# Kernel optimization log

Hardware: AMD Instinct MI355X
Metric: run time of the kernel (lower is better)

Reference implementation:

```python
import jax, jax.numpy as jnp
import numpy as np


def setup_inputs() -> dict:
    key = jax.random.key(0)
    ks = jax.random.split(key, 6)
    B, T, H, L, V = 8, 100, 1024, 512, 32000
    x = jax.random.normal(ks[0], (B, T, H), dtype=jnp.float32)
    attn_dist = jax.random.normal(ks[1], (B, T, L), dtype=jnp.float32)
    enc_input = jax.random.randint(ks[2], (B, L), 0, V, dtype=jnp.int32)
    W_vocab = jax.random.normal(ks[3], (H, V), dtype=jnp.float32) * (1.0 / np.sqrt(H))
    b_vocab = jnp.zeros((V,), dtype=jnp.float32)
    w_gen = jax.random.normal(ks[4], (H, 1), dtype=jnp.float32) * (1.0 / np.sqrt(H))
    b_gen = jnp.zeros((1,), dtype=jnp.float32)
    return {"x": x, "attn_dist": attn_dist, "enc_input": enc_input,
            "W_vocab": W_vocab, "b_vocab": b_vocab, "w_gen": w_gen, "b_gen": b_gen}


def reference(x, attn_dist, enc_input, W_vocab, b_vocab, w_gen, b_gen):
    B, T, H = x.shape
    L = attn_dist.shape[-1]
    V = W_vocab.shape[-1]
    # generation gate: sigmoid(x @ w_gen + b_gen) -> [B, T, 1]
    p_gen = jax.nn.sigmoid(jnp.einsum('bth,ho->bto', x, w_gen) + b_gen)
    # vocab distribution: softmax over vocab of the projection -> [B, T, V]
    vocab_dist = jax.nn.softmax(jnp.einsum('bth,hv->btv', x, W_vocab) + b_vocab, axis=-1)
    vocab_dist = p_gen * vocab_dist
    # copy distribution over encoder positions -> [B, T, L]
    copy_dist = (1.0 - p_gen) * jax.nn.softmax(attn_dist, axis=-1)
    # scatter-add copy probabilities into vocab slots (duplicates accumulate)
    vd = vocab_dist.reshape(B * T, V)
    cd = copy_dist.reshape(B * T, L)
    idx = jnp.broadcast_to(enc_input[:, None, :], (B, T, L)).reshape(B * T, L)
    rows = jnp.arange(B * T, dtype=jnp.int32)[:, None]
    combined = vd.at[rows, idx].add(cd)
    return jnp.log(combined).reshape(B, T, V)
```

## Files before the change

kernel.cpp:

```cpp
#include <hip/hip_runtime.h>
#include <math.h>

#define BB 8
#define TT 100
#define HH 1024
#define LL 512
#define VV 32000
#define NROWS (BB*TT)
#define MPAD 896
#define NMT 7
#define NNT 250
#define NWG (NMT*NNT)

typedef __bf16 bf16x8 __attribute__((ext_vector_type(8)));
typedef __bf16 bf16x4 __attribute__((ext_vector_type(4)));
typedef float f32x4 __attribute__((ext_vector_type(4)));

__device__ __forceinline__ void gload16(const void* g, void* l) {
  __builtin_amdgcn_global_load_lds(
      (const __attribute__((address_space(1))) unsigned int*)g,
      (__attribute__((address_space(3))) unsigned int*)l, 16, 0, 0);
}

__global__ __launch_bounds__(256) void k_cvt_x(const float* __restrict__ x,
                                               __bf16* __restrict__ xb) {
  int idx = blockIdx.x * 256 + threadIdx.x;
  int row = (idx * 4) >> 10;
  bf16x4 v;
  if (row < NROWS) {
    float4 f = ((const float4*)x)[idx];
    v[0] = (__bf16)f.x; v[1] = (__bf16)f.y; v[2] = (__bf16)f.z; v[3] = (__bf16)f.w;
  } else {
    v[0] = v[1] = v[2] = v[3] = (__bf16)0.f;
  }
  ((bf16x4*)xb)[idx] = v;
}

__global__ __launch_bounds__(256) void k_cvt_wT(const float* __restrict__ W,
                                                __bf16* __restrict__ Wtb) {
  __shared__ float T[32][257];
  int n0 = blockIdx.x * 256;
  int kt = blockIdx.y;
  int tid = threadIdx.x;
#pragma unroll
  for (int i = 0; i < 32; ++i)
    T[i][tid] = W[(size_t)(kt * 32 + i) * VV + n0 + tid];
  __syncthreads();
  int cq = tid & 3;
  int cl = tid >> 2;
  __bf16* base = Wtb + ((size_t)kt * VV + n0) * 32;
#pragma unroll
  for (int g = 0; g < 4; ++g) {
    int col = g * 64 + cl;
    bf16x8 v;
#pragma unroll
    for (int j = 0; j < 8; ++j) v[j] = (__bf16)T[cq * 8 + j][col];
    *(bf16x8*)(base + (size_t)col * 32 + cq * 8) = v;
  }
}

__global__ __launch_bounds__(256) void k_pgen_copy(
    const float* __restrict__ x, const float* __restrict__ attn,
    const float* __restrict__ w_gen, const float* __restrict__ b_gen,
    float* __restrict__ p_gen, float* __restrict__ copy_dist,
    float* __restrict__ rsum) {
  int r = blockIdx.x;
  int tid = threadIdx.x;
  __shared__ float red[4];
  if (tid == 0) rsum[r] = 0.f;

  float d = 0.f;
  for (int h = tid; h < HH; h += 256) d += x[(size_t)r * HH + h] * w_gen[h];
#pragma unroll
  for (int o = 32; o > 0; o >>= 1) d += __shfl_down(d, o, 64);
  if ((tid & 63) == 0) red[tid >> 6] = d;
  __syncthreads();
  float dot = red[0] + red[1] + red[2] + red[3];
  float p = 1.f / (1.f + __expf(-(dot + b_gen[0])));
  if (tid == 0) p_gen[r] = p;

  float a0 = attn[(size_t)r * LL + tid];
  float a1 = attn[(size_t)r * LL + 256 + tid];
  float m = fmaxf(a0, a1);
#pragma unroll
  for (int o = 32; o > 0; o >>= 1) m = fmaxf(m, __shfl_down(m, o, 64));
  __syncthreads();
  if ((tid & 63) == 0) red[tid >> 6] = m;
  __syncthreads();
  float M = fmaxf(fmaxf(red[0], red[1]), fmaxf(red[2], red[3]));
  float e0 = __expf(a0 - M), e1 = __expf(a1 - M);
  float s = e0 + e1;
#pragma unroll
  for (int o = 32; o > 0; o >>= 1) s += __shfl_down(s, o, 64);
  __syncthreads();
  if ((tid & 63) == 0) red[tid >> 6] = s;
  __syncthreads();
  float S = red[0] + red[1] + red[2] + red[3];
  float scale = (1.f - p) / S;
  copy_dist[(size_t)r * LL + tid] = e0 * scale;
  copy_dist[(size_t)r * LL + 256 + tid] = e1 * scale;
}

__global__ __launch_bounds__(256) void k_gemm_mfma(
    const __bf16* __restrict__ Xb, const __bf16* __restrict__ Wtb,
    const float* __restrict__ bias, float* __restrict__ out,
    float* __restrict__ rsum) {
  __shared__ __align__(16) __bf16 As[2][128 * 32];
  __shared__ __align__(16) __bf16 Bs[2][128 * 32];
  int tid = threadIdx.x;
  int lane = tid & 63, wave = tid >> 6;
  int wr = wave >> 1, wc = wave & 1;
  int l15 = lane & 15, quad = lane >> 4;

  int lid = blockIdx.x;
  int xcd = lid & 7, sub = lid >> 3;
  const int q = NWG >> 3, rr = NWG & 7;
  int wg = (xcd < rr) ? (xcd * (q + 1) + sub)
                      : (rr * (q + 1) + (xcd - rr) * q + sub);
  int m0 = (wg % NMT) * 128;
  int n0 = (wg / NMT) * 128;

  f32x4 acc[4][4];
#pragma unroll
  for (int mi = 0; mi < 4; ++mi)
#pragma unroll
    for (int ni = 0; ni < 4; ++ni) acc[mi][ni] = (f32x4){0.f, 0.f, 0.f, 0.f};

  int r0 = wave * 32;
  const __bf16* aptr0 = Xb + (size_t)(m0 + r0 + (lane >> 2)) * HH + (lane & 3) * 8;
  const __bf16* aptr1 = aptr0 + (size_t)16 * HH;
  const size_t bstep = (size_t)VV * 32;
  const __bf16* bptr0 = Wtb + (size_t)(n0 + r0 + (lane >> 2)) * 32 + (lane & 3) * 8;
  const __bf16* bptr1 = bptr0 + (size_t)16 * 32;

  __bf16* lA0[2] = {&As[0][r0 * 32], &As[1][r0 * 32]};
  __bf16* lA1[2] = {&As[0][(r0 + 16) * 32], &As[1][(r0 + 16) * 32]};
  __bf16* lB0[2] = {&Bs[0][r0 * 32], &Bs[1][r0 * 32]};
  __bf16* lB1[2] = {&Bs[0][(r0 + 16) * 32], &Bs[1][(r0 + 16) * 32]};

  gload16(aptr0, lA0[0]);
  gload16(aptr1, lA1[0]);
  gload16(bptr0, lB0[0]);
  gload16(bptr1, lB1[0]);

  for (int it = 0; it < 32; ++it) {
    int cur = it & 1;
    __syncthreads();
    if (it + 1 < 32) {
      int ko = (it + 1) * 32;
      size_t bo = (size_t)(it + 1) * bstep;
      int nxt = cur ^ 1;
      gload16(aptr0 + ko, lA0[nxt]);
      gload16(aptr1 + ko, lA1[nxt]);
      gload16(bptr0 + bo, lB0[nxt]);
      gload16(bptr1 + bo, lB1[nxt]);
    }
    const __bf16* Ab = As[cur];
    const __bf16* Bb = Bs[cur];
    bf16x8 af[4], bfg[4];
#pragma unroll
    for (int mi = 0; mi < 4; ++mi)
      af[mi] = *(const bf16x8*)&Ab[(wr * 64 + mi * 16 + l15) * 32 + quad * 8];
#pragma unroll
    for (int ni = 0; ni < 4; ++ni)
      bfg[ni] = *(const bf16x8*)&Bb[(wc * 64 + ni * 16 + l15) * 32 + quad * 8];
#pragma unroll
    for (int mi = 0; mi < 4; ++mi)
#pragma unroll
      for (int ni = 0; ni < 4; ++ni)
        acc[mi][ni] = __builtin_amdgcn_mfma_f32_16x16x32_bf16(af[mi], bfg[ni], acc[mi][ni], 0, 0, 0);
  }

  float bv4[4];
#pragma unroll
  for (int ni = 0; ni < 4; ++ni) bv4[ni] = bias[n0 + wc * 64 + ni * 16 + l15];

#pragma unroll
  for (int mi = 0; mi < 4; ++mi) {
#pragma unroll
    for (int rg = 0; rg < 4; ++rg) {
      int row = m0 + wr * 64 + mi * 16 + quad * 4 + rg;
      bool valid = row < NROWS;
      float esum = 0.f;
#pragma unroll
      for (int ni = 0; ni < 4; ++ni) {
        int col = n0 + wc * 64 + ni * 16 + l15;
        float v = acc[mi][ni][rg] + bv4[ni];
        if (valid) out[(size_t)row * VV + col] = v;
        esum += __expf(v);
      }
#pragma unroll
      for (int o = 8; o > 0; o >>= 1) esum += __shfl_down(esum, o, 16);
      if (l15 == 0 && valid) atomicAdd(&rsum[row], esum);
    }
  }
}

__global__ __launch_bounds__(256) void k_affine(
    float* __restrict__ out, const float* __restrict__ p_gen,
    const float* __restrict__ rsum) {
  int r = blockIdx.y;
  int c = (blockIdx.x * 256 + threadIdx.x) * 4;
  if (c >= VV) return;
  float logc = __logf(p_gen[r] / rsum[r]);
  float4 v = *(float4*)&out[(size_t)r * VV + c];
  v.x += logc; v.y += logc; v.z += logc; v.w += logc;
  *(float4*)&out[(size_t)r * VV + c] = v;
}

__global__ __launch_bounds__(256) void k_scatter_fix(
    float* __restrict__ out, const int* __restrict__ enc,
    const float* __restrict__ copy) {
  __shared__ int hkey[1024];
  __shared__ float hval[1024];
  int r = blockIdx.x, tid = threadIdx.x;
  float* row = out + (size_t)r * VV;
  for (int i = tid; i < 1024; i += 256) { hkey[i] = -1; hval[i] = 0.f; }
  __syncthreads();
  int b = r / TT;
  for (int j = tid; j < LL; j += 256) {
    int v = enc[(size_t)b * LL + j];
    float cv = copy[(size_t)r * LL + j];
    unsigned h = ((unsigned)v * 2654435761u) & 1023u;
    while (true) {
      int prev = atomicCAS(&hkey[h], -1, v);
      if (prev == -1 || prev == v) { atomicAdd(&hval[h], cv); break; }
      h = (h + 1) & 1023u;
    }
  }
  __syncthreads();
  for (int h = tid; h < 1024; h += 256) {
    int col = hkey[h];
    if (col >= 0) {
      float stored = row[col];
      row[col] = __logf(__expf(stored) + hval[h]);
    }
  }
}

extern "C" void kernel_launch(void* const* d_in, const int* in_sizes, int n_in,
                              void* d_out, int out_size, void* d_ws, size_t ws_size,
                              hipStream_t stream) {
  const float* x    = (const float*)d_in[0];
  const float* attn = (const float*)d_in[1];
  const int*   enc  = (const int*)d_in[2];
  const float* Wv   = (const float*)d_in[3];
  const float* bv   = (const float*)d_in[4];
  const float* wgen = (const float*)d_in[5];
  const float* bg   = (const float*)d_in[6];
  float* out = (float*)d_out;
  float* ws = (float*)d_ws;

  float* p_gen = ws;
  float* rsum  = ws + 1024;
  float* copy  = ws + 2048;
  __bf16* xb = (__bf16*)(ws + 2048 + NROWS * LL);
  __bf16* Wt = (__bf16*)((char*)xb + (size_t)MPAD * HH * 2);

  k_cvt_x<<<MPAD * HH / 4 / 256, 256, 0, stream>>>(x, xb);
  dim3 gw(VV / 256, HH / 32);
  k_cvt_wT<<<gw, 256, 0, stream>>>(Wv, Wt);
  k_pgen_copy<<<NROWS, 256, 0, stream>>>(x, attn, wgen, bg, p_gen, copy, rsum);
  k_gemm_mfma<<<NWG, 256, 0, stream>>>(xb, Wt, bv, out, rsum);
  dim3 ga((VV + 1023) / 1024, NROWS);
  k_affine<<<ga, 256, 0, stream>>>(out, p_gen, rsum);
  k_scatter_fix<<<NROWS, 256, 0, stream>>>(out, enc, copy);
}
```

Measured before the change: 368.6 us.

## Triple-buffer GEMM LDS stages with vmcnt waits and XOR-swizzled LDS layout

Replaces the double-buffered K loop of the MFMA vocab GEMM with a three-stage LDS ring. Two tiles are kept in flight, and explicit s_waitcnt vmcnt plus a barrier wait only for the oldest load. It also XOR-swizzles the 16-byte chunk position in each LDS row on both the global-to-LDS write and the fragment read, to cut bank conflicts. Together these aim to hide global load latency and LDS conflicts, at the cost of 50% more shared memory per block and hand-managed wait counts that must match the load ordering.

```diff
diff --git a/kernel.cpp b/kernel.cpp
--- a/kernel.cpp
+++ b/kernel.cpp
@@ -105,8 +105,8 @@
     const __bf16* __restrict__ Xb, const __bf16* __restrict__ Wtb,
     const float* __restrict__ bias, float* __restrict__ out,
     float* __restrict__ rsum) {
-  __shared__ __align__(16) __bf16 As[2][128 * 32];
-  __shared__ __align__(16) __bf16 Bs[2][128 * 32];
+  __shared__ __align__(16) __bf16 As[3][128 * 32];
+  __shared__ __align__(16) __bf16 Bs[3][128 * 32];
   int tid = threadIdx.x;
   int lane = tid & 63, wave = tid >> 6;
   int wr = wave >> 1, wc = wave & 1;
@@ -127,49 +127,60 @@
     for (int ni = 0; ni < 4; ++ni) acc[mi][ni] = (f32x4){0.f, 0.f, 0.f, 0.f};
 
   int r0 = wave * 32;
-  const __bf16* aptr0 = Xb + (size_t)(m0 + r0 + (lane >> 2)) * HH + (lane & 3) * 8;
+  int lr = lane >> 2;
+  int chunk = (lane & 3) ^ ((lr >> 1) & 3);
+  const __bf16* aptr0 = Xb + (size_t)(m0 + r0 + lr) * HH + chunk * 8;
   const __bf16* aptr1 = aptr0 + (size_t)16 * HH;
   const size_t bstep = (size_t)VV * 32;
-  const __bf16* bptr0 = Wtb + (size_t)(n0 + r0 + (lane >> 2)) * 32 + (lane & 3) * 8;
+  const __bf16* bptr0 = Wtb + (size_t)(n0 + r0 + lr) * 32 + chunk * 8;
   const __bf16* bptr1 = bptr0 + (size_t)16 * 32;
 
-  __bf16* lA0[2] = {&As[0][r0 * 32], &As[1][r0 * 32]};
-  __bf16* lA1[2] = {&As[0][(r0 + 16) * 32], &As[1][(r0 + 16) * 32]};
-  __bf16* lB0[2] = {&Bs[0][r0 * 32], &Bs[1][r0 * 32]};
-  __bf16* lB1[2] = {&Bs[0][(r0 + 16) * 32], &Bs[1][(r0 + 16) * 32]};
-
-  gload16(aptr0, lA0[0]);
-  gload16(aptr1, lA1[0]);
-  gload16(bptr0, lB0[0]);
-  gload16(bptr1, lB1[0]);
-
-  for (int it = 0; it < 32; ++it) {
-    int cur = it & 1;
-    __syncthreads();
-    if (it + 1 < 32) {
-      int ko = (it + 1) * 32;
-      size_t bo = (size_t)(it + 1) * bstep;
-      int nxt = cur ^ 1;
-      gload16(aptr0 + ko, lA0[nxt]);
-      gload16(aptr1 + ko, lA1[nxt]);
-      gload16(bptr0 + bo, lB0[nxt]);
-      gload16(bptr1 + bo, lB1[nxt]);
-    }
-    const __bf16* Ab = As[cur];
-    const __bf16* Bb = Bs[cur];
-    bf16x8 af[4], bfg[4];
-#pragma unroll
-    for (int mi = 0; mi < 4; ++mi)
-      af[mi] = *(const bf16x8*)&Ab[(wr * 64 + mi * 16 + l15) * 32 + quad * 8];
-#pragma unroll
-    for (int ni = 0; ni < 4; ++ni)
-      bfg[ni] = *(const bf16x8*)&Bb[(wc * 64 + ni * 16 + l15) * 32 + quad * 8];
-#pragma unroll
-    for (int mi = 0; mi < 4; ++mi)
-#pragma unroll
-      for (int ni = 0; ni < 4; ++ni)
-        acc[mi][ni] = __builtin_amdgcn_mfma_f32_16x16x32_bf16(af[mi], bfg[ni], acc[mi][ni], 0, 0, 0);
-  }
+  int sw8 = (quad ^ ((l15 >> 1) & 3)) * 8;
+
+#define STAGE(it, buf) do {                                          \
+    gload16(aptr0 + (size_t)(it) * 32, &As[buf][r0 * 32]);           \
+    gload16(aptr1 + (size_t)(it) * 32, &As[buf][(r0 + 16) * 32]);    \
+    gload16(bptr0 + (size_t)(it) * bstep, &Bs[buf][r0 * 32]);        \
+    gload16(bptr1 + (size_t)(it) * bstep, &Bs[buf][(r0 + 16) * 32]); \
+    __builtin_amdgcn_sched_barrier(0);                               \
+  } while (0)
+
+#define SYNCW(n) do {                                          \
+    asm volatile("s_waitcnt vmcnt(" #n ")" ::: "memory");      \
+    __builtin_amdgcn_sched_barrier(0);                         \
+    __builtin_amdgcn_s_barrier();                              \
+    __builtin_amdgcn_sched_barrier(0);                         \
+  } while (0)
+
+#define COMPUTE(buf) do {                                                     \
+    const __bf16* Ab = As[buf];                                               \
+    const __bf16* Bb = Bs[buf];                                               \
+    bf16x8 af[4], bfg[4];                                                     \
+    _Pragma("unroll")                                                         \
+    for (int mi = 0; mi < 4; ++mi)                                            \
+      af[mi] = *(const bf16x8*)&Ab[(wr * 64 + mi * 16 + l15) * 32 + sw8];     \
+    _Pragma("unroll")                                                         \
+    for (int ni = 0; ni < 4; ++ni)                                            \
+      bfg[ni] = *(const bf16x8*)&Bb[(wc * 64 + ni * 16 + l15) * 32 + sw8];    \
+    _Pragma("unroll")                                                         \
+    for (int mi = 0; mi < 4; ++mi)                                            \
+      _Pragma("unroll")                                                       \
+      for (int ni = 0; ni < 4; ++ni)                                          \
+        acc[mi][ni] = __builtin_amdgcn_mfma_f32_16x16x32_bf16(                \
+            af[mi], bfg[ni], acc[mi][ni], 0, 0, 0);                           \
+  } while (0)
+
+  STAGE(0, 0);
+  STAGE(1, 1);
+  for (int itb = 0; itb < 30; itb += 3) {
+    SYNCW(4); STAGE(itb + 2, 2); COMPUTE(0);
+    SYNCW(4); STAGE(itb + 3, 0); COMPUTE(1);
+    SYNCW(4); STAGE(itb + 4, 1); COMPUTE(2);
+  }
+  SYNCW(4);
+  COMPUTE(0);
+  SYNCW(0);
+  COMPUTE(1);
 
   float bv4[4];
 #pragma unroll
@@ -194,6 +205,9 @@
       if (l15 == 0 && valid) atomicAdd(&rsum[row], esum);
     }
   }
+#undef STAGE
+#undef SYNCW
+#undef COMPUTE
 }
 
 __global__ __launch_bounds__(256) void k_affine(
```

Result: slower. 380.5 us (+3.2%).
